# Kernel tuning notes

Measured on AMD Instinct MI355X. Metric: run time of the kernel, lower is better.

## Reference

```python
import jax, jax.numpy as jnp
import numpy as np

LATENT_DIM = 512
ASSET_DIM = 8192


def setup_inputs() -> dict:
    key = jax.random.key(0)
    ks = jax.random.split(key, 7)
    d = LATENT_DIM
    s = 1.0 / np.sqrt(d)  # torch Linear default init scale (uniform bound)
    z = jax.random.normal(ks[0], (ASSET_DIM, d), dtype=jnp.float32)
    Wq = jax.random.uniform(ks[1], (d, d), jnp.float32, -s, s)
    Wk = jax.random.uniform(ks[2], (d, d), jnp.float32, -s, s)
    Wv = jax.random.uniform(ks[3], (d, d), jnp.float32, -s, s)
    bq = jax.random.uniform(ks[4], (d,), jnp.float32, -s, s)
    bk = jax.random.uniform(ks[5], (d,), jnp.float32, -s, s)
    bv = jax.random.uniform(ks[6], (d,), jnp.float32, -s, s)
    return {"z": z, "Wq": Wq, "bq": bq, "Wk": Wk, "bk": bk, "Wv": Wv, "bv": bv}


def reference(z, Wq, bq, Wk, bk, Wv, bv):
    # z: (N, D). Single-head self-attention over assets.
    d = z.shape[-1]
    scale = d ** (-0.5)
    q = z @ Wq.T + bq          # (N, D)
    k = z @ Wk.T + bk          # (N, D)
    v = z @ Wv.T + bv          # (N, D)
    scores = jnp.einsum('nd,md->nm', q, k) * scale   # (N, N)
    attn = jax.nn.softmax(scores, axis=-1)
    # Original does attn[:, :, None] * v[None] then sum(dim=1); identical math:
    h = attn @ v               # (N, D)
    return h
```

## Files before the change

kernel.cpp:

```cpp
#include <hip/hip_runtime.h>
#include <hip/hip_bf16.h>
#include <stdint.h>

#define D 512
#define N 8192

typedef __attribute__((ext_vector_type(8))) short short8;
typedef __attribute__((ext_vector_type(4))) float f32x4;

static __device__ __forceinline__ unsigned short f2bf(float f) {
  unsigned int u = __builtin_bit_cast(unsigned int, f);
  u += 0x7fffu + ((u >> 16) & 1u);
  return (unsigned short)(u >> 16);
}
static __device__ __forceinline__ float bf2f(unsigned short s) {
  unsigned int u = ((unsigned int)s) << 16;
  return __builtin_bit_cast(float, u);
}

typedef const __attribute__((address_space(1))) unsigned int* gas_ptr;
typedef __attribute__((address_space(3))) unsigned int* las_ptr;
static __device__ __forceinline__ void gload_lds16(const void* g, void* l) {
  __builtin_amdgcn_global_load_lds((gas_ptr)g, (las_ptr)l, 16, 0, 0);
}

__global__ void cast_z_k(const float* __restrict__ z, unsigned short* __restrict__ zb) {
  int i = blockIdx.x * 256 + threadIdx.x;
  const int n4 = N * D / 4;
  for (; i < n4; i += gridDim.x * 256) {
    float4 v = ((const float4*)z)[i];
    ushort4 o = { f2bf(v.x), f2bf(v.y), f2bf(v.z), f2bf(v.w) };
    ((ushort4*)zb)[i] = o;
  }
}

__global__ void cast_w_k(const float* __restrict__ Wq, const float* __restrict__ Wk,
                         const float* __restrict__ Wv, const float* __restrict__ bq,
                         const float* __restrict__ bk, const float* __restrict__ bv,
                         unsigned short* __restrict__ wb, float* __restrict__ bqkv) {
  const float scale = 0.044194173824159216f;
  int i = blockIdx.x * 256 + threadIdx.x;
  const int per = D * D / 4;
  if (i < 3 * per) {
    int sec = i / per;
    int w4 = i - sec * per;
    const float* W = sec == 0 ? Wq : (sec == 1 ? Wk : Wv);
    float s = sec == 0 ? scale : 1.0f;
    float4 v = ((const float4*)W)[w4];
    ushort4 o = { f2bf(v.x * s), f2bf(v.y * s), f2bf(v.z * s), f2bf(v.w * s) };
    ((ushort4*)wb)[sec * per + w4] = o;
  }
  if (i < 3 * D) {
    int sec = i >> 9, j = i & (D - 1);
    const float* b = sec == 0 ? bq : (sec == 1 ? bk : bv);
    bqkv[i] = b[j] * (sec == 0 ? scale : 1.0f);
  }
}

__global__ __launch_bounds__(256) void proj_qkv(
    const unsigned short* __restrict__ A,
    const unsigned short* __restrict__ B,
    const float* __restrict__ bias,
    unsigned short* __restrict__ o0, unsigned short* __restrict__ o1,
    unsigned short* __restrict__ o2) {
  __shared__ unsigned short Ash[2][128 * 64];
  __shared__ unsigned short Bsh[2][128 * 64];

  const int t = threadIdx.x;
  const int w = t >> 6, lane = t & 63;
  const int bid = blockIdx.x;
  const int swz = (bid & 7) * 96 + (bid >> 3);
  const int tm = swz / 12, tn = swz - tm * 12;
  const int row0 = tm * 128, col0 = tn * 128;

  const int srow = t >> 3;
  const int scol = ((t & 7) ^ ((t >> 3) & 7)) * 8;
  const unsigned short* Ab = A + (size_t)(row0 + srow) * D + scol;
  const unsigned short* Bb = B + (size_t)(col0 + srow) * D + scol;
  const int ldsbase = (w * 64) * 8;

  const int l15 = lane & 15, lhi = lane >> 4, lx = lane & 7;
  const int wr = w >> 1, wc = w & 1;
  const int arow = (wr * 64 + l15) * 64;
  const int brow = (wc * 64 + l15) * 64;
  const int ko0 = ((0 + lhi) ^ lx) * 8;
  const int ko1 = ((4 + lhi) ^ lx) * 8;

  f32x4 acc[4][4] = {};

  auto stage = [&](int buf, int k0) {
    const unsigned short* a = Ab + k0;
    const unsigned short* b = Bb + k0;
    unsigned short* la = &Ash[buf][ldsbase];
    unsigned short* lb = &Bsh[buf][ldsbase];
#pragma unroll
    for (int i = 0; i < 4; ++i) {
      gload_lds16(a + (size_t)(i * 32) * D, la + i * 2048);
      gload_lds16(b + (size_t)(i * 32) * D, lb + i * 2048);
    }
  };

  stage(0, 0);
  asm volatile("s_waitcnt vmcnt(0)" ::: "memory");
  __syncthreads();
  int cur = 0;
  for (int kt = 0; kt < 8; ++kt) {
    if (kt + 1 < 8) stage(cur ^ 1, (kt + 1) * 64);
    const unsigned short* As = Ash[cur];
    const unsigned short* Bs = Bsh[cur];
#pragma unroll
    for (int ks = 0; ks < 2; ++ks) {
      const int ko = ks ? ko1 : ko0;
      short8 af[4], bg[4];
#pragma unroll
      for (int rf = 0; rf < 4; ++rf)
        af[rf] = *(const short8*)(As + arow + rf * (16 * 64) + ko);
#pragma unroll
      for (int cf = 0; cf < 4; ++cf)
        bg[cf] = *(const short8*)(Bs + brow + cf * (16 * 64) + ko);
#pragma unroll
      for (int rf = 0; rf < 4; ++rf)
#pragma unroll
        for (int cf = 0; cf < 4; ++cf)
          acc[rf][cf] = __builtin_amdgcn_mfma_f32_16x16x32_bf16(af[rf], bg[cf], acc[rf][cf], 0, 0, 0);
    }
    asm volatile("s_waitcnt vmcnt(0)" ::: "memory");
    __syncthreads();
    cur ^= 1;
  }

  const int r0g = row0 + wr * 64;
  const int c0g = col0 + wc * 64;
  const int sec = col0 >> 9;
#pragma unroll
  for (int cf = 0; cf < 4; ++cf) {
    const int c = c0g + cf * 16 + l15;
    const int cj = c & (D - 1);
    const float bb = bias[c];
#pragma unroll
    for (int rf = 0; rf < 4; ++rf) {
      const int r = r0g + rf * 16 + lhi * 4;
      f32x4 v = acc[rf][cf];
      if (sec == 0) {
#pragma unroll
        for (int g = 0; g < 4; ++g) o0[(size_t)(r + g) * D + cj] = f2bf(v[g] + bb);
      } else if (sec == 1) {
#pragma unroll
        for (int g = 0; g < 4; ++g) o1[(size_t)(r + g) * D + cj] = f2bf(v[g] + bb);
      } else {
        ushort4 o = { f2bf(v[0] + bb), f2bf(v[1] + bb), f2bf(v[2] + bb), f2bf(v[3] + bb) };
        *(ushort4*)(o2 + (size_t)cj * N + r) = o;
      }
    }
  }
}

#define STAGE8(buf, kt, LDB)                                                \
  do {                                                                      \
    const unsigned short* a_ = Ab + (size_t)(kt) * 64;                      \
    const unsigned short* b_ = Bb + (size_t)(kt) * 64;                      \
    unsigned short* la_ = &Ash[buf][0];                                     \
    unsigned short* lb_ = &Bsh[buf][0];                                     \
    gload_lds16(a_, la_ + ldst);                                            \
    gload_lds16(a_ + (size_t)64 * (LDB), la_ + 4096 + ldst);                \
    gload_lds16(a_ + (size_t)128 * (LDB), la_ + 8192 + ldst);               \
    gload_lds16(a_ + (size_t)192 * (LDB), la_ + 12288 + ldst);              \
    gload_lds16(b_, lb_ + ldst);                                            \
    gload_lds16(b_ + (size_t)64 * (LDB), lb_ + 4096 + ldst);                \
    gload_lds16(b_ + (size_t)128 * (LDB), lb_ + 8192 + ldst);               \
    gload_lds16(b_ + (size_t)192 * (LDB), lb_ + 12288 + ldst);              \
  } while (0)

#define RDA(kk, mh)                                                          \
  do {                                                                       \
    _Pragma("unroll") for (int fm = 0; fm < 4; ++fm) {                       \
      const unsigned short* p_ = &Ash[kk][aRowB + (mh) * 4096 + fm * 1024];  \
      af[fm][0] = *(const short8*)(p_ + sl0);                                \
      af[fm][1] = *(const short8*)(p_ + sl1);                                \
    }                                                                        \
  } while (0)

#define RDB(kk, nh)                                                          \
  do {                                                                       \
    _Pragma("unroll") for (int fn = 0; fn < 2; ++fn) {                       \
      const unsigned short* p_ = &Bsh[kk][bRowB + (nh) * 2048 + fn * 1024];  \
      bf[fn][0] = *(const short8*)(p_ + sl0);                                \
      bf[fn][1] = *(const short8*)(p_ + sl1);                                \
    }                                                                        \
  } while (0)

#define MMA(mh, nh)                                                          \
  do {                                                                       \
    __builtin_amdgcn_s_setprio(1);                                           \
    _Pragma("unroll") for (int ks = 0; ks < 2; ++ks)                         \
      _Pragma("unroll") for (int fm = 0; fm < 4; ++fm)                       \
        _Pragma("unroll") for (int fn = 0; fn < 2; ++fn)                     \
          acc[(mh) * 4 + fm][(nh) * 2 + fn] =                                \
              __builtin_amdgcn_mfma_f32_16x16x32_bf16(                       \
                  af[fm][ks], bf[fn][ks], acc[(mh) * 4 + fm][(nh) * 2 + fn], \
                  0, 0, 0);                                                  \
    __builtin_amdgcn_s_setprio(0);                                           \
  } while (0)

#define BARLG()                                         \
  do {                                                  \
    __builtin_amdgcn_s_barrier();                       \
    asm volatile("s_waitcnt lgkmcnt(0)" ::: "memory");  \
    __builtin_amdgcn_sched_barrier(0);                  \
  } while (0)

#define VMDRAIN() asm volatile("s_waitcnt vmcnt(0)" ::: "memory")
#define POSTBAR() __builtin_amdgcn_s_barrier()

#define EIGHT_PHASE_LOOP(NI, KT0, LDB)                              \
  STAGE8(0, (KT0), LDB);                                            \
  VMDRAIN();                                                        \
  __builtin_amdgcn_s_barrier();                                     \
  for (int i = 0; i < (NI); ++i) {                                  \
    RDA(0, 0); RDB(0, 0);                                           \
    STAGE8(1, (KT0) + 2 * i + 1, LDB);                              \
    BARLG(); MMA(0, 0); POSTBAR();                                  \
    RDB(0, 1);                                                      \
    BARLG(); MMA(0, 1); POSTBAR();                                  \
    RDA(0, 1);                                                      \
    BARLG(); MMA(1, 1); POSTBAR();                                  \
    RDB(0, 0);                                                      \
    VMDRAIN();                                                      \
    BARLG(); MMA(1, 0); POSTBAR();                                  \
    RDA(1, 0); RDB(1, 0);                                           \
    if (i + 1 < (NI)) STAGE8(0, (KT0) + 2 * i + 2, LDB);            \
    BARLG(); MMA(0, 0); POSTBAR();                                  \
    RDB(1, 1);                                                      \
    BARLG(); MMA(0, 1); POSTBAR();                                  \
    RDA(1, 1);                                                      \
    BARLG(); MMA(1, 1); POSTBAR();                                  \
    RDB(1, 0);                                                      \
    if (i + 1 < (NI)) VMDRAIN();                                    \
    BARLG(); MMA(1, 0); POSTBAR();                                  \
  }

__global__ __launch_bounds__(512, 2) void qk_exp_8ph(
    const unsigned short* __restrict__ A,
    const unsigned short* __restrict__ B,
    unsigned short* __restrict__ P,
    float* __restrict__ lpart) {
  __shared__ unsigned short Ash[2][256 * 64];
  __shared__ unsigned short Bsh[2][256 * 64];

  const int t = threadIdx.x;
  const int w = t >> 6, lane = t & 63;
  const int bid = blockIdx.x;
  const int swz = (bid & 7) * 128 + (bid >> 3);
  const int tm = swz >> 5, tn = swz & 31;
  const int row0 = tm * 256, col0 = tn * 256;

  const int wr = w >> 2, wc = w & 3;
  const int l15 = lane & 15, lhi = lane >> 4, lx = lane & 7;

  const int sr = t >> 3;
  const int ss = ((t & 7) ^ (sr & 7)) * 8;
  const unsigned short* Ab = A + (size_t)(row0 + sr) * D + ss;
  const unsigned short* Bb = B + (size_t)(col0 + sr) * D + ss;
  const int ldst = t * 8;

  const int aRowB = (wr * 128 + l15) * 64;
  const int bRowB = (wc * 64 + l15) * 64;
  const int sl0 = ((0 + lhi) ^ lx) * 8;
  const int sl1 = ((4 + lhi) ^ lx) * 8;

  f32x4 acc[8][4] = {};
  short8 af[4][2], bf[2][2];

  EIGHT_PHASE_LOOP(4, 0, D)

#pragma unroll
  for (int fm = 0; fm < 8; ++fm) {
    const int r = row0 + wr * 128 + fm * 16 + lhi * 4;
    float rs[4] = {0.f, 0.f, 0.f, 0.f};
#pragma unroll
    for (int fn = 0; fn < 4; ++fn) {
      const int c = col0 + wc * 64 + fn * 16 + l15;
      f32x4 v = acc[fm][fn];
#pragma unroll
      for (int g = 0; g < 4; ++g) {
        unsigned short us = f2bf(__expf(v[g]));
        P[(size_t)(r + g) * N + c] = us;
        rs[g] += bf2f(us);
      }
    }
#pragma unroll
    for (int g = 0; g < 4; ++g) {
      float s = rs[g];
      s += __shfl_xor(s, 1);
      s += __shfl_xor(s, 2);
      s += __shfl_xor(s, 4);
      s += __shfl_xor(s, 8);
      if (l15 == 0) lpart[(size_t)(tn * 4 + wc) * N + r + g] = s;
    }
  }
}

__global__ __launch_bounds__(512, 2) void pv_8ph(
    const unsigned short* __restrict__ A,
    const unsigned short* __restrict__ B,
    unsigned short* __restrict__ Opart,
    float* __restrict__ outF) {
  __shared__ unsigned short Ash[2][256 * 64];
  __shared__ unsigned short Bsh[2][256 * 64];

  const int t = threadIdx.x;
  const int w = t >> 6, lane = t & 63;
  const int bid = blockIdx.x;
  const int swz = (bid & 7) * 32 + (bid >> 3);
  const int sp = swz >> 6;
  const int idx = swz & 63;
  const int tm = idx >> 1, tn = idx & 1;
  const int row0 = tm * 256, col0 = tn * 256;
  const int kt0 = sp * 32;

  const int wr = w >> 2, wc = w & 3;
  const int l15 = lane & 15, lhi = lane >> 4, lx = lane & 7;

  const int sr = t >> 3;
  const int ss = ((t & 7) ^ (sr & 7)) * 8;
  const unsigned short* Ab = A + (size_t)(row0 + sr) * N + ss;
  const unsigned short* Bb = B + (size_t)(col0 + sr) * N + ss;
  const int ldst = t * 8;

  const int aRowB = (wr * 128 + l15) * 64;
  const int bRowB = (wc * 64 + l15) * 64;
  const int sl0 = ((0 + lhi) ^ lx) * 8;
  const int sl1 = ((4 + lhi) ^ lx) * 8;

  f32x4 acc[8][4] = {};
  short8 af[4][2], bf[2][2];

  EIGHT_PHASE_LOOP(16, kt0, N)

  if (sp < 3) {
    unsigned short* op = Opart + (size_t)sp * ((size_t)N * D);
#pragma unroll
    for (int fm = 0; fm < 8; ++fm) {
      const int r = row0 + wr * 128 + fm * 16 + lhi * 4;
#pragma unroll
      for (int fn = 0; fn < 4; ++fn) {
        const int c = col0 + wc * 64 + fn * 16 + l15;
        f32x4 v = acc[fm][fn];
#pragma unroll
        for (int g = 0; g < 4; ++g) op[(size_t)(r + g) * D + c] = f2bf(v[g]);
      }
    }
  } else {
#pragma unroll
    for (int fm = 0; fm < 8; ++fm) {
      const int r = row0 + wr * 128 + fm * 16 + lhi * 4;
#pragma unroll
      for (int fn = 0; fn < 4; ++fn) {
        const int c = col0 + wc * 64 + fn * 16 + l15;
        f32x4 v = acc[fm][fn];
#pragma unroll
        for (int g = 0; g < 4; ++g) outF[(size_t)(r + g) * D + c] = v[g];
      }
    }
  }
}

__global__ void linv_k(const float* __restrict__ lpart, float* __restrict__ linv) {
  const int m = blockIdx.x * 256 + threadIdx.x;
  float s = 0.f;
  for (int i = 0; i < 128; ++i) s += lpart[(size_t)i * N + m];
  linv[m] = 1.0f / s;
}

__global__ void reduce_k(const unsigned short* __restrict__ Opart,
                         const float* __restrict__ linv, float* __restrict__ out) {
  const int i = blockIdx.x * 256 + threadIdx.x;
  const int m = i >> 7;
  const float li = linv[m];
  const size_t nd = (size_t)N * D;
  ushort4 a = ((const ushort4*)Opart)[i];
  ushort4 b = ((const ushort4*)(Opart + nd))[i];
  ushort4 c = ((const ushort4*)(Opart + 2 * nd))[i];
  float4 o = ((float4*)out)[i];
  o.x = (bf2f(a.x) + bf2f(b.x) + bf2f(c.x) + o.x) * li;
  o.y = (bf2f(a.y) + bf2f(b.y) + bf2f(c.y) + o.y) * li;
  o.z = (bf2f(a.z) + bf2f(b.z) + bf2f(c.z) + o.z) * li;
  o.w = (bf2f(a.w) + bf2f(b.w) + bf2f(c.w) + o.w) * li;
  ((float4*)out)[i] = o;
}

extern "C" void kernel_launch(void* const* d_in, const int* in_sizes, int n_in,
                              void* d_out, int out_size, void* d_ws, size_t ws_size,
                              hipStream_t stream) {
  const float* z  = (const float*)d_in[0];
  const float* Wq = (const float*)d_in[1];
  const float* bq = (const float*)d_in[2];
  const float* Wk = (const float*)d_in[3];
  const float* bk = (const float*)d_in[4];
  const float* Wv = (const float*)d_in[5];
  const float* bv = (const float*)d_in[6];
  float* out = (float*)d_out;

  char* ws = (char*)d_ws;
  unsigned short* zb = (unsigned short*)(ws + 0);
  unsigned short* qb = (unsigned short*)(ws + 8388608);
  unsigned short* kb = (unsigned short*)(ws + 16777216);
  unsigned short* vT = (unsigned short*)(ws + 25165824);
  unsigned short* wb = (unsigned short*)(ws + 33554432);
  float* linv       = (float*)(ws + 33554432);
  float* bqkv       = (float*)(ws + 35127296);
  float* lpart      = (float*)(ws + 35133440);
  unsigned short* P = (unsigned short*)(ws + 39327744);
  unsigned short* Opart = (unsigned short*)(ws + 0);

  cast_z_k<<<dim3(2048), dim3(256), 0, stream>>>(z, zb);
  cast_w_k<<<dim3(768), dim3(256), 0, stream>>>(Wq, Wk, Wv, bq, bk, bv, wb, bqkv);

  proj_qkv<<<dim3(768), dim3(256), 0, stream>>>(zb, wb, bqkv, qb, kb, vT);

  qk_exp_8ph<<<dim3(1024), dim3(512), 0, stream>>>(qb, kb, P, lpart);

  linv_k<<<dim3(32), dim3(256), 0, stream>>>(lpart, linv);

  pv_8ph<<<dim3(256), dim3(512), 0, stream>>>(P, vT, Opart, out);

  reduce_k<<<dim3(4096), dim3(256), 0, stream>>>(Opart, linv, out);
}
```

Measured before the change: 227.2 us.

## Halve K-tile to 32 in QK-exp kernel to cut LDS footprint

Rewrites the QK^T+exp kernel's pipelined main loop to stage K in 32-wide slices instead of 64, halving the shared-memory buffers and the A/B fragment registers. The swizzle and read offsets change to match the narrower rows, and the loop runs twice as many iterations. The intent is to lower LDS and register use so more blocks stay resident and latency is hidden better. In exchange it adds twice as many barriers and global-load rounds per unit of work, and each MMA phase has less work to overlap with them.

```diff
diff --git a/kernel.cpp b/kernel.cpp
--- a/kernel.cpp
+++ b/kernel.cpp
@@ -239,13 +239,73 @@
     BARLG(); MMA(1, 0); POSTBAR();                                  \
   }
 
+#define STAGE4_K32(buf, kt)                                          \
+  do {                                                               \
+    const unsigned short* a_ = Ab + (size_t)(kt) * 32;               \
+    const unsigned short* b_ = Bb + (size_t)(kt) * 32;               \
+    gload_lds16(a_, &Ash[buf][ldst]);                                \
+    gload_lds16(a_ + (size_t)128 * D, &Ash[buf][4096 + ldst]);       \
+    gload_lds16(b_, &Bsh[buf][ldst]);                                \
+    gload_lds16(b_ + (size_t)128 * D, &Bsh[buf][4096 + ldst]);       \
+  } while (0)
+
+#define RDA_K32(kk, mh)                                                       \
+  do {                                                                        \
+    _Pragma("unroll") for (int fm = 0; fm < 4; ++fm)                          \
+      af[fm] = *(const short8*)&Ash[kk][aRowB + (mh) * 2048 + fm * 512 + sl]; \
+  } while (0)
+
+#define RDB_K32(kk, nh)                                                       \
+  do {                                                                        \
+    _Pragma("unroll") for (int fn = 0; fn < 2; ++fn)                          \
+      bf[fn] = *(const short8*)&Bsh[kk][bRowB + (nh) * 1024 + fn * 512 + sl]; \
+  } while (0)
+
+#define MMA_K32(mh, nh)                                                      \
+  do {                                                                       \
+    __builtin_amdgcn_s_setprio(1);                                           \
+    _Pragma("unroll") for (int fm = 0; fm < 4; ++fm)                         \
+      _Pragma("unroll") for (int fn = 0; fn < 2; ++fn)                       \
+        acc[(mh) * 4 + fm][(nh) * 2 + fn] =                                  \
+            __builtin_amdgcn_mfma_f32_16x16x32_bf16(                         \
+                af[fm], bf[fn], acc[(mh) * 4 + fm][(nh) * 2 + fn], 0, 0, 0); \
+    __builtin_amdgcn_s_setprio(0);                                           \
+  } while (0)
+
+#define EIGHT_PHASE_LOOP_K32(NI)                                    \
+  STAGE4_K32(0, 0);                                                 \
+  VMDRAIN();                                                        \
+  __builtin_amdgcn_s_barrier();                                     \
+  for (int i = 0; i < (NI); ++i) {                                  \
+    RDA_K32(0, 0); RDB_K32(0, 0);                                   \
+    STAGE4_K32(1, 2 * i + 1);                                       \
+    BARLG(); MMA_K32(0, 0); POSTBAR();                              \
+    RDB_K32(0, 1);                                                  \
+    BARLG(); MMA_K32(0, 1); POSTBAR();                              \
+    RDA_K32(0, 1);                                                  \
+    BARLG(); MMA_K32(1, 1); POSTBAR();                              \
+    RDB_K32(0, 0);                                                  \
+    VMDRAIN();                                                      \
+    BARLG(); MMA_K32(1, 0); POSTBAR();                              \
+    RDA_K32(1, 0); RDB_K32(1, 0);                                   \
+    if (i + 1 < (NI)) STAGE4_K32(0, 2 * i + 2);                     \
+    BARLG(); MMA_K32(0, 0); POSTBAR();                              \
+    RDB_K32(1, 1);                                                  \
+    BARLG(); MMA_K32(0, 1); POSTBAR();                              \
+    RDA_K32(1, 1);                                                  \
+    BARLG(); MMA_K32(1, 1); POSTBAR();                              \
+    RDB_K32(1, 0);                                                  \
+    if (i + 1 < (NI)) VMDRAIN();                                    \
+    BARLG(); MMA_K32(1, 0); POSTBAR();                              \
+  }
+
 __global__ __launch_bounds__(512, 2) void qk_exp_8ph(
     const unsigned short* __restrict__ A,
     const unsigned short* __restrict__ B,
     unsigned short* __restrict__ P,
     float* __restrict__ lpart) {
-  __shared__ unsigned short Ash[2][256 * 64];
-  __shared__ unsigned short Bsh[2][256 * 64];
+  __shared__ unsigned short Ash[2][256 * 32];
+  __shared__ unsigned short Bsh[2][256 * 32];
 
   const int t = threadIdx.x;
   const int w = t >> 6, lane = t & 63;
@@ -255,23 +315,22 @@
   const int row0 = tm * 256, col0 = tn * 256;
 
   const int wr = w >> 2, wc = w & 3;
-  const int l15 = lane & 15, lhi = lane >> 4, lx = lane & 7;
-
-  const int sr = t >> 3;
-  const int ss = ((t & 7) ^ (sr & 7)) * 8;
+  const int l15 = lane & 15, lhi = lane >> 4;
+
+  const int sr = t >> 2;
+  const int ss = ((t & 3) ^ (sr & 3)) * 8;
   const unsigned short* Ab = A + (size_t)(row0 + sr) * D + ss;
   const unsigned short* Bb = B + (size_t)(col0 + sr) * D + ss;
   const int ldst = t * 8;
 
-  const int aRowB = (wr * 128 + l15) * 64;
-  const int bRowB = (wc * 64 + l15) * 64;
-  const int sl0 = ((0 + lhi) ^ lx) * 8;
-  const int sl1 = ((4 + lhi) ^ lx) * 8;
+  const int aRowB = (wr * 128 + l15) * 32;
+  const int bRowB = (wc * 64 + l15) * 32;
+  const int sl = (lhi ^ (l15 & 3)) * 8;
 
   f32x4 acc[8][4] = {};
-  short8 af[4][2], bf[2][2];
-
-  EIGHT_PHASE_LOOP(4, 0, D)
+  short8 af[4], bf[2];
+
+  EIGHT_PHASE_LOOP_K32(8)
 
 #pragma unroll
   for (int fm = 0; fm < 8; ++fm) {
```

Result: no change. 231.3 us (+1.8%).

## Process two column tiles per QK block and overlap P stores with second GEMM

Applied to the files above, without the earlier changes.

The QK^T+exp kernel now handles two adjacent 256-column tiles per block and launches half as many blocks. The exp'd bf16 results of the first tile are packed into registers, then written to global memory interleaved with the MMA phases of the second tile's GEMM. The vmcnt wait is relaxed so these stores do not stall the next tile's loads. The aim is to hide the P-store epilogue behind matrix math, at the cost of extra registers (pk array) and possible occupancy pressure, plus fewer blocks in the grid.

```diff
diff --git a/kernel.cpp b/kernel.cpp
--- a/kernel.cpp
+++ b/kernel.cpp
@@ -210,6 +210,7 @@
   } while (0)
 
 #define VMDRAIN() asm volatile("s_waitcnt vmcnt(0)" ::: "memory")
+#define VM12()    asm volatile("s_waitcnt vmcnt(12)" ::: "memory")
 #define POSTBAR() __builtin_amdgcn_s_barrier()
 
 #define EIGHT_PHASE_LOOP(NI, KT0, LDB)                              \
@@ -239,6 +240,18 @@
     BARLG(); MMA(1, 0); POSTBAR();                                  \
   }
 
+#define ST4(ci)                                                       \
+  do {                                                                \
+    const int fm_ = (ci) >> 2, fn_ = (ci) & 3;                        \
+    const size_t r_ = row0 + wr * 128 + fm_ * 16 + lhi * 4;           \
+    const int c_ = col0_0 + wc * 64 + fn_ * 16 + l15;                 \
+    unsigned lo_ = pk[fm_][fn_].x, hi_ = pk[fm_][fn_].y;              \
+    P[(r_ + 0) * N + c_] = (unsigned short)lo_;                       \
+    P[(r_ + 1) * N + c_] = (unsigned short)(lo_ >> 16);               \
+    P[(r_ + 2) * N + c_] = (unsigned short)hi_;                       \
+    P[(r_ + 3) * N + c_] = (unsigned short)(hi_ >> 16);               \
+  } while (0)
+
 __global__ __launch_bounds__(512, 2) void qk_exp_8ph(
     const unsigned short* __restrict__ A,
     const unsigned short* __restrict__ B,
@@ -250,9 +263,11 @@
   const int t = threadIdx.x;
   const int w = t >> 6, lane = t & 63;
   const int bid = blockIdx.x;
-  const int swz = (bid & 7) * 128 + (bid >> 3);
-  const int tm = swz >> 5, tn = swz & 31;
-  const int row0 = tm * 256, col0 = tn * 256;
+  const int swz = (bid & 7) * 64 + (bid >> 3);
+  const int tm = swz >> 4, tnp = swz & 15;
+  const int row0 = tm * 256;
+  const int tn0 = tnp * 2, col0_0 = tn0 * 256;
+  const int tn1 = tn0 + 1, col0_1 = tn1 * 256;
 
   const int wr = w >> 2, wc = w & 3;
   const int l15 = lane & 15, lhi = lane >> 4, lx = lane & 7;
@@ -260,7 +275,6 @@
   const int sr = t >> 3;
   const int ss = ((t & 7) ^ (sr & 7)) * 8;
   const unsigned short* Ab = A + (size_t)(row0 + sr) * D + ss;
-  const unsigned short* Bb = B + (size_t)(col0 + sr) * D + ss;
   const int ldst = t * 8;
 
   const int aRowB = (wr * 128 + l15) * 64;
@@ -268,10 +282,14 @@
   const int sl0 = ((0 + lhi) ^ lx) * 8;
   const int sl1 = ((4 + lhi) ^ lx) * 8;
 
+  short8 af[4][2], bf[2][2];
   f32x4 acc[8][4] = {};
-  short8 af[4][2], bf[2][2];
-
-  EIGHT_PHASE_LOOP(4, 0, D)
+  uint2 pk[8][4];
+
+  {
+    const unsigned short* Bb = B + (size_t)(col0_0 + sr) * D + ss;
+    EIGHT_PHASE_LOOP(4, 0, D)
+  }
 
 #pragma unroll
   for (int fm = 0; fm < 8; ++fm) {
@@ -279,14 +297,13 @@
     float rs[4] = {0.f, 0.f, 0.f, 0.f};
 #pragma unroll
     for (int fn = 0; fn < 4; ++fn) {
-      const int c = col0 + wc * 64 + fn * 16 + l15;
       f32x4 v = acc[fm][fn];
-#pragma unroll
-      for (int g = 0; g < 4; ++g) {
-        unsigned short us = f2bf(__expf(v[g]));
-        P[(size_t)(r + g) * N + c] = us;
-        rs[g] += bf2f(us);
-      }
+      unsigned short u0 = f2bf(__expf(v[0])), u1 = f2bf(__expf(v[1]));
+      unsigned short u2 = f2bf(__expf(v[2])), u3 = f2bf(__expf(v[3]));
+      pk[fm][fn].x = (unsigned)u0 | ((unsigned)u1 << 16);
+      pk[fm][fn].y = (unsigned)u2 | ((unsigned)u3 << 16);
+      rs[0] += bf2f(u0); rs[1] += bf2f(u1); rs[2] += bf2f(u2); rs[3] += bf2f(u3);
+      acc[fm][fn] = (f32x4){0.f, 0.f, 0.f, 0.f};
     }
 #pragma unroll
     for (int g = 0; g < 4; ++g) {
@@ -295,7 +312,64 @@
       s += __shfl_xor(s, 2);
       s += __shfl_xor(s, 4);
       s += __shfl_xor(s, 8);
-      if (l15 == 0) lpart[(size_t)(tn * 4 + wc) * N + r + g] = s;
+      if (l15 == 0) lpart[(size_t)(tn0 * 4 + wc) * N + r + g] = s;
+    }
+  }
+
+  {
+    const unsigned short* Bb = B + (size_t)(col0_1 + sr) * D + ss;
+    STAGE8(0, 0, D);
+    VMDRAIN();
+    __builtin_amdgcn_s_barrier();
+    for (int i = 0; i < 4; ++i) {
+      RDA(0, 0); RDB(0, 0);
+      STAGE8(1, 2 * i + 1, D);
+      ST4(i * 8 + 0);
+      BARLG(); MMA(0, 0); POSTBAR();
+      RDB(0, 1); ST4(i * 8 + 1);
+      BARLG(); MMA(0, 1); POSTBAR();
+      RDA(0, 1); ST4(i * 8 + 2);
+      BARLG(); MMA(1, 1); POSTBAR();
+      RDB(0, 0); ST4(i * 8 + 3);
+      VM12();
+      BARLG(); MMA(1, 0); POSTBAR();
+      RDA(1, 0); RDB(1, 0);
+      if (i + 1 < 4) STAGE8(0, 2 * i + 2, D);
+      ST4(i * 8 + 4);
+      BARLG(); MMA(0, 0); POSTBAR();
+      RDB(1, 1); ST4(i * 8 + 5);
+      BARLG(); MMA(0, 1); POSTBAR();
+      RDA(1, 1); ST4(i * 8 + 6);
+      BARLG(); MMA(1, 1); POSTBAR();
+      RDB(1, 0); ST4(i * 8 + 7);
+      if (i + 1 < 4) VM12();
+      BARLG(); MMA(1, 0); POSTBAR();
+    }
+  }
+
+#pragma unroll
+  for (int fm = 0; fm < 8; ++fm) {
+    const int r = row0 + wr * 128 + fm * 16 + lhi * 4;
+    float rs[4] = {0.f, 0.f, 0.f, 0.f};
+#pragma unroll
+    for (int fn = 0; fn < 4; ++fn) {
+      const int c = col0_1 + wc * 64 + fn * 16 + l15;
+      f32x4 v = acc[fm][fn];
+#pragma unroll
+      for (int g = 0; g < 4; ++g) {
+        unsigned short us = f2bf(__expf(v[g]));
+        P[(size_t)(r + g) * N + c] = us;
+        rs[g] += bf2f(us);
+      }
+    }
+#pragma unroll
+    for (int g = 0; g < 4; ++g) {
+      float s = rs[g];
+      s += __shfl_xor(s, 1);
+      s += __shfl_xor(s, 2);
+      s += __shfl_xor(s, 4);
+      s += __shfl_xor(s, 8);
+      if (l15 == 0) lpart[(size_t)(tn1 * 4 + wc) * N + r + g] = s;
     }
   }
 }
@@ -418,7 +492,7 @@
 
   proj_qkv<<<dim3(768), dim3(256), 0, stream>>>(zb, wb, bqkv, qb, kb, vT);
 
-  qk_exp_8ph<<<dim3(1024), dim3(512), 0, stream>>>(qb, kb, P, lpart);
+  qk_exp_8ph<<<dim3(512), dim3(512), 0, stream>>>(qb, kb, P, lpart);
 
   linv_k<<<dim3(32), dim3(256), 0, stream>>>(lpart, linv);
 
```

After: 287.2 us. 1.26x slower.
